# Kernel optimization log

Measured on AMD Instinct MI355X. Metric: run time of the kernel, lower is better.

The kernel has to match this reference:

```python
import jax, jax.numpy as jnp
import numpy as np

D_MODEL = 1024
N_HEAD = 16


def setup_inputs() -> dict:
    key = jax.random.key(0)
    ks = jax.random.split(key, 11)
    B, T, D = 4, 2048, D_MODEL
    s = 1.0 / np.sqrt(D)
    inp = {
        "q": jax.random.normal(ks[0], (B, T, D), jnp.float32),
        "k": jax.random.normal(ks[1], (B, T, D), jnp.float32),
        "v": jax.random.normal(ks[2], (B, T, D), jnp.float32),
        "wq": jax.random.normal(ks[3], (D, D), jnp.float32) * s,
        "bq": jnp.zeros((D,), jnp.float32),
        "wk": jax.random.normal(ks[4], (D, D), jnp.float32) * s,
        "bk": jnp.zeros((D,), jnp.float32),
        "wv": jax.random.normal(ks[5], (D, D), jnp.float32) * s,
        "bv": jnp.zeros((D,), jnp.float32),
        "wo": jax.random.normal(ks[6], (D, D), jnp.float32) * s,
        "bo": jnp.zeros((D,), jnp.float32),
    }
    return inp


def reference(q, k, v, wq, bq, wk, bk, wv, bv, wo, bo):
    B, T, D = q.shape
    H = N_HEAD
    hd = D // H  # head dim
    # torch nn.Linear: y = x @ W.T + b
    qh = (q @ wq.T + bq).reshape(B, T, H, hd).transpose(0, 2, 1, 3)  # [B,H,T,hd]
    kh = (k @ wk.T + bk).reshape(B, T, H, hd).transpose(0, 2, 1, 3)
    vh = (v @ wv.T + bv).reshape(B, T, H, hd).transpose(0, 2, 1, 3)
    scale = 1.0 / jnp.sqrt(jnp.asarray(hd, qh.dtype))
    score = jnp.einsum("bhqd,bhkd->bhqk", qh, kh) * scale  # [B,H,T,T]
    causal = jnp.tril(jnp.ones((T, T), dtype=bool))
    score = jnp.where(causal, score, jnp.asarray(-jnp.inf, score.dtype))
    attn = jax.nn.softmax(score, axis=-1)
    out = jnp.einsum("bhqk,bhkd->bhqd", attn, vh)  # [B,H,T,hd]
    out = out.transpose(0, 2, 1, 3).reshape(B, T, D)
    return out @ wo.T + bo
```

## Files before the change

### kernel.cpp

```cpp
#include <hip/hip_runtime.h>
#include <hip/hip_bf16.h>

#define D_MODEL 1024
#define N_HEAD  16
#define HD      64
#define T_SEQ   2048
#define B_SZ    4
#define M_ROWS  (B_SZ * T_SEQ)

typedef __bf16 bf16;
typedef __bf16 bf16x4 __attribute__((ext_vector_type(4)));
typedef __bf16 bf16x8 __attribute__((ext_vector_type(8)));
typedef float  floatx4 __attribute__((ext_vector_type(4)));

__device__ __forceinline__ floatx4 fzero4() {
    floatx4 z = {0.f, 0.f, 0.f, 0.f};
    return z;
}

__device__ __forceinline__ void async_ld16(const void* g, void* l) {
    __builtin_amdgcn_global_load_lds(
        (const __attribute__((address_space(1))) void*)g,
        (__attribute__((address_space(3))) void*)l,
        16, 0, 0);
}

struct CvtArgs {
    const float* s[7];
    bf16* d[7];
    int n[7];
};

__global__ __launch_bounds__(256) void cvt7_kernel(CvtArgs a)
{
    const float* src = a.s[blockIdx.y];
    bf16* dst = a.d[blockIdx.y];
    int n8 = a.n[blockIdx.y];
    int i = blockIdx.x * blockDim.x + threadIdx.x;
    int stride = gridDim.x * blockDim.x;
    for (; i < n8; i += stride) {
        float4 x = ((const float4*)src)[2 * i];
        float4 y = ((const float4*)src)[2 * i + 1];
        bf16x8 o;
        o[0] = (bf16)x.x; o[1] = (bf16)x.y; o[2] = (bf16)x.z; o[3] = (bf16)x.w;
        o[4] = (bf16)y.x; o[5] = (bf16)y.y; o[6] = (bf16)y.z; o[7] = (bf16)y.w;
        ((bf16x8*)dst)[i] = o;
    }
}

template <int OMODE>
__global__ __launch_bounds__(256) void gemm_bf16(
    const bf16* __restrict__ A0, const bf16* __restrict__ W0,
    const float* __restrict__ b0v, void* __restrict__ O0, float scl0,
    const bf16* __restrict__ A1, const bf16* __restrict__ W1,
    const float* __restrict__ b1v, void* __restrict__ O1, float scl1)
{
    __shared__ bf16 ldsA[128 * 64];
    __shared__ bf16 ldsW[128 * 64];

    const bf16* A     = blockIdx.z ? A1 : A0;
    const bf16* W     = blockIdx.z ? W1 : W0;
    const float* bias = blockIdx.z ? b1v : b0v;
    void* Out         = blockIdx.z ? O1 : O0;
    const float scl   = blockIdx.z ? scl1 : scl0;

    const int tid  = threadIdx.x;
    const int wave = tid >> 6, lane = tid & 63;
    const int quad = lane >> 4, l15 = lane & 15;
    const int wr = wave >> 1, wc = wave & 1;
    const int m0 = blockIdx.y * 128, n0 = blockIdx.x * 128;

    floatx4 acc[4][4];
#pragma unroll
    for (int i = 0; i < 4; ++i)
#pragma unroll
        for (int j = 0; j < 4; ++j) acc[i][j] = fzero4();

    const int ro = lane >> 3;
    const int gc = (lane & 7) ^ ro;
    const bf16* gA = A + (size_t)(m0 + wave * 32 + ro) * 1024 + gc * 8;
    const bf16* gW = W + (size_t)(n0 + wave * 32 + ro) * 1024 + gc * 8;

    for (int kt = 0; kt < 16; ++kt) {
        __syncthreads();
#pragma unroll
        for (int j = 0; j < 4; ++j)
            async_ld16((const void*)(gA + kt * 64 + j * 8 * 1024), &ldsA[(wave * 32 + j * 8) * 64]);
#pragma unroll
        for (int j = 0; j < 4; ++j)
            async_ld16((const void*)(gW + kt * 64 + j * 8 * 1024), &ldsW[(wave * 32 + j * 8) * 64]);
        __syncthreads();

#pragma unroll
        for (int ks = 0; ks < 2; ++ks) {
            const int pos = ((ks * 4 + quad) ^ (l15 & 7)) * 8;
            bf16x8 af[4], bw[4];
#pragma unroll
            for (int i = 0; i < 4; ++i)
                af[i] = *(const bf16x8*)(&ldsA[(wr * 64 + i * 16 + l15) * 64 + pos]);
#pragma unroll
            for (int j = 0; j < 4; ++j)
                bw[j] = *(const bf16x8*)(&ldsW[(wc * 64 + j * 16 + l15) * 64 + pos]);
#pragma unroll
            for (int i = 0; i < 4; ++i)
#pragma unroll
                for (int j = 0; j < 4; ++j)
                    acc[i][j] = __builtin_amdgcn_mfma_f32_16x16x32_bf16(af[i], bw[j], acc[i][j], 0, 0, 0);
        }
    }

#pragma unroll
    for (int i = 0; i < 4; ++i) {
#pragma unroll
        for (int j = 0; j < 4; ++j) {
#pragma unroll
            for (int r = 0; r < 4; ++r) {
                int m = m0 + wr * 64 + i * 16 + quad * 4 + r;
                int n = n0 + wc * 64 + j * 16 + l15;
                float val = (acc[i][j][r] + bias[n]) * scl;
                if (OMODE == 2) {
                    ((float*)Out)[(size_t)m * 1024 + n] = val;
                } else {
                    int b = m >> 11, t = m & 2047;
                    int h = n >> 6,  d = n & 63;
                    size_t addr;
                    if (OMODE == 0)
                        addr = ((size_t)(b * N_HEAD + h) * T_SEQ + t) * HD + d;
                    else
                        addr = ((size_t)(b * N_HEAD + h) * HD + d) * T_SEQ + t;
                    ((bf16*)Out)[addr] = (bf16)val;
                }
            }
        }
    }
}

__global__ __launch_bounds__(256, 2) void attn_kernel(
    const bf16* __restrict__ Qh, const bf16* __restrict__ Kh,
    const bf16* __restrict__ Vt, bf16* __restrict__ AO)
{
    __shared__ bf16 Ks[128 * 64];
    __shared__ bf16 Vts[64 * 128];
    __shared__ bf16 Ps[128 * 72];

    const int tid  = threadIdx.x;
    const int wave = tid >> 6, lane = tid & 63;
    const int quad = lane >> 4, l15 = lane & 15;
    const int bh = blockIdx.y;
    const size_t base = (size_t)bh * T_SEQ * HD;
    const int bb = bh >> 4, hh = bh & 15;

    const int kro = lane >> 3;
    const int kgc = (lane & 7) ^ kro;
    const bf16* kgbase = Kh + base + (size_t)(wave * 32 + kro) * HD + kgc * 8;
    const int vrow_lo = lane >> 4;
    const int vchunk  = lane & 15;

    const bf16* vgbase[4];
    bf16* kdst[4];
    bf16* vdst[4];
#pragma unroll
    for (int j = 0; j < 4; ++j) {
        int d = wave * 16 + j * 4 + vrow_lo;
        int gcv = vchunk ^ (d & 15);
        vgbase[j] = Vt + base + (size_t)d * T_SEQ + gcv * 8;
        vdst[j]   = &Vts[d * 128 + vchunk * 8];
        kdst[j]   = &Ks[(wave * 32 + j * 8 + kro) * 64 + (lane & 7) * 8];
    }

    for (int phase = 0; phase < 2; ++phase) {
        const int qt = phase ? blockIdx.x : 15 - blockIdx.x;

        bf16x8 qf[2][2];
        const bf16* qbase = Qh + base + (size_t)(qt * 128 + wave * 32) * HD;
#pragma unroll
        for (int ti = 0; ti < 2; ++ti)
#pragma unroll
            for (int ks = 0; ks < 2; ++ks)
                qf[ti][ks] = *(const bf16x8*)(qbase + (ti * 16 + l15) * HD + ks * 32 + quad * 8);

        bf16x8 kreg[4], vreg[4];
#pragma unroll
        for (int j = 0; j < 4; ++j)
            kreg[j] = *(const bf16x8*)(kgbase + (size_t)(j * 8) * HD);
#pragma unroll
        for (int j = 0; j < 4; ++j)
            vreg[j] = *(const bf16x8*)(vgbase[j]);

        float mrow[2] = {-1e30f, -1e30f}, lrow[2] = {0.f, 0.f};
        floatx4 oacc[2][4];
#pragma unroll
        for (int ti = 0; ti < 2; ++ti)
#pragma unroll
            for (int nj = 0; nj < 4; ++nj) oacc[ti][nj] = fzero4();

        for (int kt = 0; kt <= qt; ++kt) {
            __syncthreads();
#pragma unroll
            for (int j = 0; j < 4; ++j) *(bf16x8*)kdst[j] = kreg[j];
#pragma unroll
            for (int j = 0; j < 4; ++j) *(bf16x8*)vdst[j] = vreg[j];
            __syncthreads();

            if (kt < qt) {
#pragma unroll
                for (int j = 0; j < 4; ++j)
                    kreg[j] = *(const bf16x8*)(kgbase + (size_t)((kt + 1) * 128 + j * 8) * HD);
#pragma unroll
                for (int j = 0; j < 4; ++j)
                    vreg[j] = *(const bf16x8*)(vgbase[j] + (kt + 1) * 128);
            }

            const bool diag = (kt == qt);
            const int lim = diag ? (2 * wave + 1) : 7;

            floatx4 sacc[2][8];
#pragma unroll
            for (int ti = 0; ti < 2; ++ti)
#pragma unroll
                for (int tj = 0; tj < 8; ++tj) sacc[ti][tj] = fzero4();
            __builtin_amdgcn_s_setprio(1);
#pragma unroll
            for (int ks = 0; ks < 2; ++ks) {
                const int pos = ((ks * 4 + quad) ^ (l15 & 7)) * 8;
#pragma unroll
                for (int tj = 0; tj < 8; ++tj) {
                    if (tj <= lim) {
                        bf16x8 kf = *(const bf16x8*)(&Ks[(tj * 16 + l15) * 64 + pos]);
                        sacc[0][tj] = __builtin_amdgcn_mfma_f32_16x16x32_bf16(kf, qf[0][ks], sacc[0][tj], 0, 0, 0);
                        sacc[1][tj] = __builtin_amdgcn_mfma_f32_16x16x32_bf16(kf, qf[1][ks], sacc[1][tj], 0, 0, 0);
                    }
                }
            }
            __builtin_amdgcn_s_setprio(0);

#pragma unroll
            for (int ti = 0; ti < 2; ++ti) {
                const int ql = wave * 32 + ti * 16 + l15;
                float mxp[4] = {-1e30f, -1e30f, -1e30f, -1e30f};
#pragma unroll
                for (int tj = 0; tj < 8; ++tj) {
                    if (tj <= lim) {
#pragma unroll
                        for (int r = 0; r < 4; ++r) {
                            float s = sacc[ti][tj][r];
                            if (diag && (tj * 16 + quad * 4 + r) > ql) s = -1e30f;
                            sacc[ti][tj][r] = s;
                            mxp[r] = fmaxf(mxp[r], s);
                        }
                    }
                }
                float mx = fmaxf(fmaxf(mxp[0], mxp[1]), fmaxf(mxp[2], mxp[3]));
                mx = fmaxf(mx, __shfl_xor(mx, 16));
                mx = fmaxf(mx, __shfl_xor(mx, 32));
                if (__any(mx > mrow[ti] + 8.0f)) {
                    float mnew  = fmaxf(mrow[ti], mx);
                    float alpha = exp2f(mrow[ti] - mnew);
                    mrow[ti] = mnew;
                    lrow[ti] *= alpha;
#pragma unroll
                    for (int r = 0; r < 4; ++r) {
                        float ar = __shfl(alpha, quad * 4 + r);
#pragma unroll
                        for (int nj = 0; nj < 4; ++nj)
                            oacc[ti][nj][r] *= ar;
                    }
                }
                float rs[4] = {0.f, 0.f, 0.f, 0.f};
#pragma unroll
                for (int tj = 0; tj < 8; ++tj) {
                    if (tj <= lim) {
#pragma unroll
                        for (int r = 0; r < 4; ++r) {
                            float p = exp2f(sacc[ti][tj][r] - mrow[ti]);
                            rs[r] += p;
                            sacc[ti][tj][r] = p;
                        }
                    }
                }
                float rsum = (rs[0] + rs[1]) + (rs[2] + rs[3]);
                rsum += __shfl_xor(rsum, 16);
                rsum += __shfl_xor(rsum, 32);
                lrow[ti] += rsum;
            }

#pragma unroll
            for (int h2 = 0; h2 < 2; ++h2) {
                if (4 * h2 > lim) break;
#pragma unroll
                for (int ti = 0; ti < 2; ++ti) {
                    const int ql = wave * 32 + ti * 16 + l15;
#pragma unroll
                    for (int tjo = 0; tjo < 4; ++tjo) {
                        int tj = 4 * h2 + tjo;
                        if (tj <= lim) {
                            bf16x4 pv;
#pragma unroll
                            for (int r = 0; r < 4; ++r) pv[r] = (bf16)sacc[ti][tj][r];
                            *(bf16x4*)(&Ps[ql * 72 + tjo * 16 + quad * 4]) = pv;
                        }
                    }
                }
#pragma unroll
                for (int ks2 = 0; ks2 < 2; ++ks2) {
                    const int gks = 2 * h2 + ks2;
                    if (diag && gks > wave) break;
                    bf16x8 pf[2];
                    pf[0] = *(const bf16x8*)(&Ps[(wave * 32 + l15) * 72 + ks2 * 32 + quad * 8]);
                    pf[1] = *(const bf16x8*)(&Ps[(wave * 32 + 16 + l15) * 72 + ks2 * 32 + quad * 8]);
                    __builtin_amdgcn_s_setprio(1);
#pragma unroll
                    for (int nj = 0; nj < 4; ++nj) {
                        int pos = ((gks * 4 + quad) ^ l15) * 8;
                        bf16x8 vf = *(const bf16x8*)(&Vts[(nj * 16 + l15) * 128 + pos]);
                        oacc[0][nj] = __builtin_amdgcn_mfma_f32_16x16x32_bf16(pf[0], vf, oacc[0][nj], 0, 0, 0);
                        oacc[1][nj] = __builtin_amdgcn_mfma_f32_16x16x32_bf16(pf[1], vf, oacc[1][nj], 0, 0, 0);
                    }
                    __builtin_amdgcn_s_setprio(0);
                }
            }
        }

#pragma unroll
        for (int ti = 0; ti < 2; ++ti) {
#pragma unroll
            for (int r = 0; r < 4; ++r) {
                float lv = __shfl(lrow[ti], quad * 4 + r);
                float rl = 1.f / lv;
                int qrow = qt * 128 + wave * 32 + ti * 16 + quad * 4 + r;
#pragma unroll
                for (int nj = 0; nj < 4; ++nj) {
                    int d = nj * 16 + l15;
                    AO[((size_t)(bb * T_SEQ + qrow)) * D_MODEL + hh * HD + d] =
                        (bf16)(oacc[ti][nj][r] * rl);
                }
            }
        }
    }
}

extern "C" void kernel_launch(void* const* d_in, const int* in_sizes, int n_in,
                              void* d_out, int out_size, void* d_ws, size_t ws_size,
                              hipStream_t stream)
{
    const float* q  = (const float*)d_in[0];
    const float* k  = (const float*)d_in[1];
    const float* v  = (const float*)d_in[2];
    const float* wq = (const float*)d_in[3];
    const float* bq = (const float*)d_in[4];
    const float* wk = (const float*)d_in[5];
    const float* bk = (const float*)d_in[6];
    const float* wv = (const float*)d_in[7];
    const float* bv = (const float*)d_in[8];
    const float* wo = (const float*)d_in[9];
    const float* bo = (const float*)d_in[10];

    char* ws  = (char*)d_ws;
    char* dob = (char*)d_out;
    const size_t MB = 1024 * 1024;

    bf16* Wqb = (bf16*)(ws);
    bf16* Wkb = (bf16*)(ws + 2 * MB);
    bf16* Wvb = (bf16*)(ws + 4 * MB);
    bf16* Vb  = (bf16*)(ws + 6 * MB);
    bf16* AO  = (bf16*)(ws + 6 * MB);
    bf16* Qh  = (bf16*)(ws + 22 * MB);
    bf16* Kh  = (bf16*)(ws + 38 * MB);
    bf16* Wob = (bf16*)(ws + 54 * MB);
    bf16* Qb  = (bf16*)(dob);
    bf16* Kb  = (bf16*)(dob + 16 * MB);
    bf16* Vt  = (bf16*)(dob);

    const int NQ8 = M_ROWS * D_MODEL / 8;
    const int NW8 = D_MODEL * D_MODEL / 8;
    const float QSCALE = 0.18033688011112042f;

    CvtArgs ca;
    ca.s[0] = q;  ca.d[0] = Qb;  ca.n[0] = NQ8;
    ca.s[1] = k;  ca.d[1] = Kb;  ca.n[1] = NQ8;
    ca.s[2] = v;  ca.d[2] = Vb;  ca.n[2] = NQ8;
    ca.s[3] = wq; ca.d[3] = Wqb; ca.n[3] = NW8;
    ca.s[4] = wk; ca.d[4] = Wkb; ca.n[4] = NW8;
    ca.s[5] = wv; ca.d[5] = Wvb; ca.n[5] = NW8;
    ca.s[6] = wo; ca.d[6] = Wob; ca.n[6] = NW8;

    hipLaunchKernelGGL(cvt7_kernel, dim3(512, 7), dim3(256), 0, stream, ca);
    hipLaunchKernelGGL((gemm_bf16<0>), dim3(8, 64, 2), dim3(256), 0, stream,
                       Qb, Wqb, bq, (void*)Qh, QSCALE,
                       Kb, Wkb, bk, (void*)Kh, 1.0f);
    hipLaunchKernelGGL((gemm_bf16<1>), dim3(8, 64, 1), dim3(256), 0, stream,
                       Vb, Wvb, bv, (void*)Vt, 1.0f,
                       Vb, Wvb, bv, (void*)Vt, 1.0f);
    hipLaunchKernelGGL(attn_kernel, dim3(8, 64), dim3(256), 0, stream, Qh, Kh, Vt, AO);
    hipLaunchKernelGGL((gemm_bf16<2>), dim3(8, 64, 1), dim3(256), 0, stream,
                       AO, Wob, bo, d_out, 1.0f,
                       AO, Wob, bo, d_out, 1.0f);
}
```

Before: 354.6 us.

## Fuse fp32-to-bf16 conversion into GEMM loads and merge QKV projections into one launch

Removes the standalone conversion kernel: the GEMMs now read fp32 activations and weights directly, convert them to bf16 in registers and store them into LDS. The Q, K and V projections are merged into a single launch with a grid z-dimension of 3. Global loads switch from async direct-to-LDS to register prefetch of the next k-tile, giving software pipelining. This avoids writing and re-reading bf16 copies of the inputs, but each GEMM block now reads fp32 data, twice the bytes of bf16, and weights are re-converted by every block that uses them.

```diff
diff --git a/kernel.cpp b/kernel.cpp
--- a/kernel.cpp
+++ b/kernel.cpp
@@ -18,51 +18,34 @@
     return z;
 }
 
-__device__ __forceinline__ void async_ld16(const void* g, void* l) {
-    __builtin_amdgcn_global_load_lds(
-        (const __attribute__((address_space(1))) void*)g,
-        (__attribute__((address_space(3))) void*)l,
-        16, 0, 0);
+__device__ __forceinline__ bf16x8 cvt8(const float4 a, const float4 b) {
+    bf16x8 o;
+    o[0] = (bf16)a.x; o[1] = (bf16)a.y; o[2] = (bf16)a.z; o[3] = (bf16)a.w;
+    o[4] = (bf16)b.x; o[5] = (bf16)b.y; o[6] = (bf16)b.z; o[7] = (bf16)b.w;
+    return o;
 }
 
-struct CvtArgs {
-    const float* s[7];
-    bf16* d[7];
-    int n[7];
+struct GemmArgs {
+    const void*  A[3];
+    const float* W[3];
+    const float* bias[3];
+    void*        Out[3];
+    float        scl[3];
+    int          omode[3];
 };
 
-__global__ __launch_bounds__(256) void cvt7_kernel(CvtArgs a)
-{
-    const float* src = a.s[blockIdx.y];
-    bf16* dst = a.d[blockIdx.y];
-    int n8 = a.n[blockIdx.y];
-    int i = blockIdx.x * blockDim.x + threadIdx.x;
-    int stride = gridDim.x * blockDim.x;
-    for (; i < n8; i += stride) {
-        float4 x = ((const float4*)src)[2 * i];
-        float4 y = ((const float4*)src)[2 * i + 1];
-        bf16x8 o;
-        o[0] = (bf16)x.x; o[1] = (bf16)x.y; o[2] = (bf16)x.z; o[3] = (bf16)x.w;
-        o[4] = (bf16)y.x; o[5] = (bf16)y.y; o[6] = (bf16)y.z; o[7] = (bf16)y.w;
-        ((bf16x8*)dst)[i] = o;
-    }
-}
-
-template <int OMODE>
-__global__ __launch_bounds__(256) void gemm_bf16(
-    const bf16* __restrict__ A0, const bf16* __restrict__ W0,
-    const float* __restrict__ b0v, void* __restrict__ O0, float scl0,
-    const bf16* __restrict__ A1, const bf16* __restrict__ W1,
-    const float* __restrict__ b1v, void* __restrict__ O1, float scl1)
+template <int AF32>
+__global__ __launch_bounds__(256, 2) void gemm_k(GemmArgs g)
 {
     __shared__ bf16 ldsA[128 * 64];
     __shared__ bf16 ldsW[128 * 64];
 
-    const bf16* A     = blockIdx.z ? A1 : A0;
-    const bf16* W     = blockIdx.z ? W1 : W0;
-    const float* bias = blockIdx.z ? b1v : b0v;
-    void* Out         = blockIdx.z ? O1 : O0;
-    const float scl   = blockIdx.z ? scl1 : scl0;
+    const int z = blockIdx.z;
+    const float* W    = g.W[z];
+    const float* bias = g.bias[z];
+    void* Out         = g.Out[z];
+    const float scl   = g.scl[z];
+    const int omode   = g.omode[z];
 
     const int tid  = threadIdx.x;
     const int wave = tid >> 6, lane = tid & 63;
@@ -77,19 +60,61 @@
         for (int j = 0; j < 4; ++j) acc[i][j] = fzero4();
 
     const int ro = lane >> 3;
-    const int gc = (lane & 7) ^ ro;
-    const bf16* gA = A + (size_t)(m0 + wave * 32 + ro) * 1024 + gc * 8;
-    const bf16* gW = W + (size_t)(n0 + wave * 32 + ro) * 1024 + gc * 8;
+    const int c8 = lane & 7;
+
+    bf16* dA = &ldsA[(wave * 32 + ro) * 64 + (c8 ^ ro) * 8];
+    bf16* dW = &ldsW[(wave * 32 + ro) * 64 + (c8 ^ ro) * 8];
+
+    const float* gW = W + (size_t)(n0 + wave * 32 + ro) * 1024 + c8 * 8;
+    const float* gAf = nullptr;
+    const bf16*  gAb = nullptr;
+    if constexpr (AF32)
+        gAf = (const float*)g.A[z] + (size_t)(m0 + wave * 32 + ro) * 1024 + c8 * 8;
+    else
+        gAb = (const bf16*)g.A[z] + (size_t)(m0 + wave * 32 + ro) * 1024 + c8 * 8;
+
+    float4 rw[4][2];
+    float4 raf[4][2];
+    bf16x8 rab[4];
+
+#pragma unroll
+    for (int j = 0; j < 4; ++j) {
+        if constexpr (AF32) {
+            raf[j][0] = *(const float4*)(gAf + (size_t)j * 8192);
+            raf[j][1] = *(const float4*)(gAf + (size_t)j * 8192 + 4);
+        } else {
+            rab[j] = *(const bf16x8*)(gAb + (size_t)j * 8192);
+        }
+        rw[j][0] = *(const float4*)(gW + (size_t)j * 8192);
+        rw[j][1] = *(const float4*)(gW + (size_t)j * 8192 + 4);
+    }
 
     for (int kt = 0; kt < 16; ++kt) {
         __syncthreads();
 #pragma unroll
-        for (int j = 0; j < 4; ++j)
-            async_ld16((const void*)(gA + kt * 64 + j * 8 * 1024), &ldsA[(wave * 32 + j * 8) * 64]);
-#pragma unroll
-        for (int j = 0; j < 4; ++j)
-            async_ld16((const void*)(gW + kt * 64 + j * 8 * 1024), &ldsW[(wave * 32 + j * 8) * 64]);
+        for (int j = 0; j < 4; ++j) {
+            if constexpr (AF32)
+                *(bf16x8*)(dA + j * 8 * 64) = cvt8(raf[j][0], raf[j][1]);
+            else
+                *(bf16x8*)(dA + j * 8 * 64) = rab[j];
+            *(bf16x8*)(dW + j * 8 * 64) = cvt8(rw[j][0], rw[j][1]);
+        }
         __syncthreads();
+
+        if (kt < 15) {
+            const int off = (kt + 1) * 64;
+#pragma unroll
+            for (int j = 0; j < 4; ++j) {
+                if constexpr (AF32) {
+                    raf[j][0] = *(const float4*)(gAf + off + (size_t)j * 8192);
+                    raf[j][1] = *(const float4*)(gAf + off + (size_t)j * 8192 + 4);
+                } else {
+                    rab[j] = *(const bf16x8*)(gAb + off + (size_t)j * 8192);
+                }
+                rw[j][0] = *(const float4*)(gW + off + (size_t)j * 8192);
+                rw[j][1] = *(const float4*)(gW + off + (size_t)j * 8192 + 4);
+            }
+        }
 
 #pragma unroll
         for (int ks = 0; ks < 2; ++ks) {
@@ -118,13 +143,13 @@
                 int m = m0 + wr * 64 + i * 16 + quad * 4 + r;
                 int n = n0 + wc * 64 + j * 16 + l15;
                 float val = (acc[i][j][r] + bias[n]) * scl;
-                if (OMODE == 2) {
+                if (omode == 2) {
                     ((float*)Out)[(size_t)m * 1024 + n] = val;
                 } else {
                     int b = m >> 11, t = m & 2047;
                     int h = n >> 6,  d = n & 63;
                     size_t addr;
-                    if (OMODE == 0)
+                    if (omode == 0)
                         addr = ((size_t)(b * N_HEAD + h) * T_SEQ + t) * HD + d;
                     else
                         addr = ((size_t)(b * N_HEAD + h) * HD + d) * T_SEQ + t;
@@ -359,40 +384,24 @@
     char* dob = (char*)d_out;
     const size_t MB = 1024 * 1024;
 
-    bf16* Wqb = (bf16*)(ws);
-    bf16* Wkb = (bf16*)(ws + 2 * MB);
-    bf16* Wvb = (bf16*)(ws + 4 * MB);
-    bf16* Vb  = (bf16*)(ws + 6 * MB);
     bf16* AO  = (bf16*)(ws + 6 * MB);
     bf16* Qh  = (bf16*)(ws + 22 * MB);
     bf16* Kh  = (bf16*)(ws + 38 * MB);
-    bf16* Wob = (bf16*)(ws + 54 * MB);
-    bf16* Qb  = (bf16*)(dob);
-    bf16* Kb  = (bf16*)(dob + 16 * MB);
     bf16* Vt  = (bf16*)(dob);
 
-    const int NQ8 = M_ROWS * D_MODEL / 8;
-    const int NW8 = D_MODEL * D_MODEL / 8;
     const float QSCALE = 0.18033688011112042f;
 
-    CvtArgs ca;
-    ca.s[0] = q;  ca.d[0] = Qb;  ca.n[0] = NQ8;
-    ca.s[1] = k;  ca.d[1] = Kb;  ca.n[1] = NQ8;
-    ca.s[2] = v;  ca.d[2] = Vb;  ca.n[2] = NQ8;
-    ca.s[3] = wq; ca.d[3] = Wqb; ca.n[3] = NW8;
-    ca.s[4] = wk; ca.d[4] = Wkb; ca.n[4] = NW8;
-    ca.s[5] = wv; ca.d[5] = Wvb; ca.n[5] = NW8;
-    ca.s[6] = wo; ca.d[6] = Wob; ca.n[6] = NW8;
-
-    hipLaunchKernelGGL(cvt7_kernel, dim3(512, 7), dim3(256), 0, stream, ca);
-    hipLaunchKernelGGL((gemm_bf16<0>), dim3(8, 64, 2), dim3(256), 0, stream,
-                       Qb, Wqb, bq, (void*)Qh, QSCALE,
-                       Kb, Wkb, bk, (void*)Kh, 1.0f);
-    hipLaunchKernelGGL((gemm_bf16<1>), dim3(8, 64, 1), dim3(256), 0, stream,
-                       Vb, Wvb, bv, (void*)Vt, 1.0f,
-                       Vb, Wvb, bv, (void*)Vt, 1.0f);
+    GemmArgs gq;
+    gq.A[0] = q; gq.W[0] = wq; gq.bias[0] = bq; gq.Out[0] = (void*)Qh; gq.scl[0] = QSCALE; gq.omode[0] = 0;
+    gq.A[1] = k; gq.W[1] = wk; gq.bias[1] = bk; gq.Out[1] = (void*)Kh; gq.scl[1] = 1.0f;   gq.omode[1] = 0;
+    gq.A[2] = v; gq.W[2] = wv; gq.bias[2] = bv; gq.Out[2] = (void*)Vt; gq.scl[2] = 1.0f;   gq.omode[2] = 1;
+
+    GemmArgs go;
+    go.A[0] = AO; go.W[0] = wo; go.bias[0] = bo; go.Out[0] = d_out; go.scl[0] = 1.0f; go.omode[0] = 2;
+    go.A[1] = AO; go.W[1] = wo; go.bias[1] = bo; go.Out[1] = d_out; go.scl[1] = 1.0f; go.omode[1] = 2;
+    go.A[2] = AO; go.W[2] = wo; go.bias[2] = bo; go.Out[2] = d_out; go.scl[2] = 1.0f; go.omode[2] = 2;
+
+    hipLaunchKernelGGL((gemm_k<1>), dim3(8, 64, 3), dim3(256), 0, stream, gq);
     hipLaunchKernelGGL(attn_kernel, dim3(8, 64), dim3(256), 0, stream, Qh, Kh, Vt, AO);
-    hipLaunchKernelGGL((gemm_bf16<2>), dim3(8, 64, 1), dim3(256), 0, stream,
-                       AO, Wob, bo, d_out, 1.0f,
-                       AO, Wob, bo, d_out, 1.0f);
+    hipLaunchKernelGGL((gemm_k<0>), dim3(8, 64, 1), dim3(256), 0, stream, go);
 }
```

Measured after the change: 450.0 us. 1.27x slower.

## Enlarge projection GEMM tiles to 256x128 with 8 waves and vectorize transposed V stores

Applied to the files above, without the earlier changes.

The templated 128x128 GEMM is replaced by a single 512-thread kernel that computes a 256x128 output tile. The output mode (head layout, transposed V layout, or fp32) is now chosen at runtime from an argument struct. Each W tile is now reused across twice as many A rows, and the block grid order is swapped so x walks M. In the transposed-V epilogue, the four row accumulators that are contiguous in t are packed into one bf16x4 store instead of four strided scalar stores. The cost is fewer blocks per launch (256 for the V and output projections), more LDS per block, and a runtime branch in the epilogue.

```diff
diff --git a/kernel.cpp b/kernel.cpp
--- a/kernel.cpp
+++ b/kernel.cpp
@@ -18,6 +18,13 @@
     return z;
 }
 
+__device__ __forceinline__ bf16x8 cvt8(const float4 a, const float4 b) {
+    bf16x8 o;
+    o[0] = (bf16)a.x; o[1] = (bf16)a.y; o[2] = (bf16)a.z; o[3] = (bf16)a.w;
+    o[4] = (bf16)b.x; o[5] = (bf16)b.y; o[6] = (bf16)b.z; o[7] = (bf16)b.w;
+    return o;
+}
+
 __device__ __forceinline__ void async_ld16(const void* g, void* l) {
     __builtin_amdgcn_global_load_lds(
         (const __attribute__((address_space(1))) void*)g,
@@ -30,7 +37,6 @@
     bf16* d[7];
     int n[7];
 };
-
 __global__ __launch_bounds__(256) void cvt7_kernel(CvtArgs a)
 {
     const float* src = a.s[blockIdx.y];
@@ -41,34 +47,37 @@
     for (; i < n8; i += stride) {
         float4 x = ((const float4*)src)[2 * i];
         float4 y = ((const float4*)src)[2 * i + 1];
-        bf16x8 o;
-        o[0] = (bf16)x.x; o[1] = (bf16)x.y; o[2] = (bf16)x.z; o[3] = (bf16)x.w;
-        o[4] = (bf16)y.x; o[5] = (bf16)y.y; o[6] = (bf16)y.z; o[7] = (bf16)y.w;
-        ((bf16x8*)dst)[i] = o;
+        ((bf16x8*)dst)[i] = cvt8(x, y);
     }
 }
 
-template <int OMODE>
-__global__ __launch_bounds__(256) void gemm_bf16(
-    const bf16* __restrict__ A0, const bf16* __restrict__ W0,
-    const float* __restrict__ b0v, void* __restrict__ O0, float scl0,
-    const bf16* __restrict__ A1, const bf16* __restrict__ W1,
-    const float* __restrict__ b1v, void* __restrict__ O1, float scl1)
+struct GemmArgs {
+    const bf16* A[2];
+    const bf16* W[2];
+    const float* bias[2];
+    void*       Out[2];
+    float       scl[2];
+    int         omode[2];
+};
+
+__global__ __launch_bounds__(512, 4) void gemm_k(GemmArgs g)
 {
-    __shared__ bf16 ldsA[128 * 64];
+    __shared__ bf16 ldsA[256 * 64];
     __shared__ bf16 ldsW[128 * 64];
 
-    const bf16* A     = blockIdx.z ? A1 : A0;
-    const bf16* W     = blockIdx.z ? W1 : W0;
-    const float* bias = blockIdx.z ? b1v : b0v;
-    void* Out         = blockIdx.z ? O1 : O0;
-    const float scl   = blockIdx.z ? scl1 : scl0;
+    const int z = blockIdx.z;
+    const bf16* A     = g.A[z];
+    const bf16* W     = g.W[z];
+    const float* bias = g.bias[z];
+    void* Out         = g.Out[z];
+    const float scl   = g.scl[z];
+    const int omode   = g.omode[z];
 
     const int tid  = threadIdx.x;
     const int wave = tid >> 6, lane = tid & 63;
     const int quad = lane >> 4, l15 = lane & 15;
     const int wr = wave >> 1, wc = wave & 1;
-    const int m0 = blockIdx.y * 128, n0 = blockIdx.x * 128;
+    const int m0 = blockIdx.x * 256, n0 = blockIdx.y * 128;
 
     floatx4 acc[4][4];
 #pragma unroll
@@ -77,18 +86,20 @@
         for (int j = 0; j < 4; ++j) acc[i][j] = fzero4();
 
     const int ro = lane >> 3;
-    const int gc = (lane & 7) ^ ro;
-    const bf16* gA = A + (size_t)(m0 + wave * 32 + ro) * 1024 + gc * 8;
-    const bf16* gW = W + (size_t)(n0 + wave * 32 + ro) * 1024 + gc * 8;
+    const int c8 = lane & 7;
+    const bf16* gA = A + (size_t)(m0 + wave * 32 + ro) * 1024 + (c8 ^ ro) * 8;
+    const bf16* gW = W + (size_t)(n0 + wave * 16 + ro) * 1024 + (c8 ^ ro) * 8;
 
     for (int kt = 0; kt < 16; ++kt) {
         __syncthreads();
 #pragma unroll
         for (int j = 0; j < 4; ++j)
-            async_ld16((const void*)(gA + kt * 64 + j * 8 * 1024), &ldsA[(wave * 32 + j * 8) * 64]);
-#pragma unroll
-        for (int j = 0; j < 4; ++j)
-            async_ld16((const void*)(gW + kt * 64 + j * 8 * 1024), &ldsW[(wave * 32 + j * 8) * 64]);
+            async_ld16((const void*)(gA + kt * 64 + (size_t)j * 8 * 1024),
+                       &ldsA[(wave * 32 + j * 8) * 64]);
+#pragma unroll
+        for (int j = 0; j < 2; ++j)
+            async_ld16((const void*)(gW + kt * 64 + (size_t)j * 8 * 1024),
+                       &ldsW[(wave * 16 + j * 8) * 64]);
         __syncthreads();
 
 #pragma unroll
@@ -113,22 +124,31 @@
     for (int i = 0; i < 4; ++i) {
 #pragma unroll
         for (int j = 0; j < 4; ++j) {
-#pragma unroll
-            for (int r = 0; r < 4; ++r) {
-                int m = m0 + wr * 64 + i * 16 + quad * 4 + r;
+            if (omode == 1) {
+                int m = m0 + wr * 64 + i * 16 + quad * 4;
                 int n = n0 + wc * 64 + j * 16 + l15;
-                float val = (acc[i][j][r] + bias[n]) * scl;
-                if (OMODE == 2) {
-                    ((float*)Out)[(size_t)m * 1024 + n] = val;
-                } else {
-                    int b = m >> 11, t = m & 2047;
-                    int h = n >> 6,  d = n & 63;
-                    size_t addr;
-                    if (OMODE == 0)
-                        addr = ((size_t)(b * N_HEAD + h) * T_SEQ + t) * HD + d;
-                    else
-                        addr = ((size_t)(b * N_HEAD + h) * HD + d) * T_SEQ + t;
-                    ((bf16*)Out)[addr] = (bf16)val;
+                int b = m >> 11, t0 = m & 2047;
+                int h = n >> 6,  d = n & 63;
+                bf16x4 pv;
+#pragma unroll
+                for (int r = 0; r < 4; ++r)
+                    pv[r] = (bf16)((acc[i][j][r] + bias[n]) * scl);
+                size_t addr = ((size_t)(b * N_HEAD + h) * HD + d) * T_SEQ + t0;
+                *(bf16x4*)(&((bf16*)Out)[addr]) = pv;
+            } else {
+#pragma unroll
+                for (int r = 0; r < 4; ++r) {
+                    int m = m0 + wr * 64 + i * 16 + quad * 4 + r;
+                    int n = n0 + wc * 64 + j * 16 + l15;
+                    float val = (acc[i][j][r] + bias[n]) * scl;
+                    if (omode == 2) {
+                        ((float*)Out)[(size_t)m * 1024 + n] = val;
+                    } else {
+                        int b = m >> 11, t = m & 2047;
+                        int h = n >> 6,  d = n & 63;
+                        size_t addr = ((size_t)(b * N_HEAD + h) * T_SEQ + t) * HD + d;
+                        ((bf16*)Out)[addr] = (bf16)val;
+                    }
                 }
             }
         }
@@ -362,11 +382,11 @@
     bf16* Wqb = (bf16*)(ws);
     bf16* Wkb = (bf16*)(ws + 2 * MB);
     bf16* Wvb = (bf16*)(ws + 4 * MB);
-    bf16* Vb  = (bf16*)(ws + 6 * MB);
-    bf16* AO  = (bf16*)(ws + 6 * MB);
-    bf16* Qh  = (bf16*)(ws + 22 * MB);
-    bf16* Kh  = (bf16*)(ws + 38 * MB);
-    bf16* Wob = (bf16*)(ws + 54 * MB);
+    bf16* Wob = (bf16*)(ws + 6 * MB);
+    bf16* Vb  = (bf16*)(ws + 8 * MB);
+    bf16* AO  = (bf16*)(ws + 8 * MB);
+    bf16* Qh  = (bf16*)(ws + 24 * MB);
+    bf16* Kh  = (bf16*)(ws + 40 * MB);
     bf16* Qb  = (bf16*)(dob);
     bf16* Kb  = (bf16*)(dob + 16 * MB);
     bf16* Vt  = (bf16*)(dob);
@@ -384,15 +404,21 @@
     ca.s[5] = wv; ca.d[5] = Wvb; ca.n[5] = NW8;
     ca.s[6] = wo; ca.d[6] = Wob; ca.n[6] = NW8;
 
+    GemmArgs gqk;
+    gqk.A[0] = Qb; gqk.W[0] = Wqb; gqk.bias[0] = bq; gqk.Out[0] = (void*)Qh; gqk.scl[0] = QSCALE; gqk.omode[0] = 0;
+    gqk.A[1] = Kb; gqk.W[1] = Wkb; gqk.bias[1] = bk; gqk.Out[1] = (void*)Kh; gqk.scl[1] = 1.0f;   gqk.omode[1] = 0;
+
+    GemmArgs gv;
+    gv.A[0] = Vb; gv.W[0] = Wvb; gv.bias[0] = bv; gv.Out[0] = (void*)Vt; gv.scl[0] = 1.0f; gv.omode[0] = 1;
+    gv.A[1] = Vb; gv.W[1] = Wvb; gv.bias[1] = bv; gv.Out[1] = (void*)Vt; gv.scl[1] = 1.0f; gv.omode[1] = 1;
+
+    GemmArgs go;
+    go.A[0] = AO; go.W[0] = Wob; go.bias[0] = bo; go.Out[0] = d_out; go.scl[0] = 1.0f; go.omode[0] = 2;
+    go.A[1] = AO; go.W[1] = Wob; go.bias[1] = bo; go.Out[1] = d_out; go.scl[1] = 1.0f; go.omode[1] = 2;
+
     hipLaunchKernelGGL(cvt7_kernel, dim3(512, 7), dim3(256), 0, stream, ca);
-    hipLaunchKernelGGL((gemm_bf16<0>), dim3(8, 64, 2), dim3(256), 0, stream,
-                       Qb, Wqb, bq, (void*)Qh, QSCALE,
-                       Kb, Wkb, bk, (void*)Kh, 1.0f);
-    hipLaunchKernelGGL((gemm_bf16<1>), dim3(8, 64, 1), dim3(256), 0, stream,
-                       Vb, Wvb, bv, (void*)Vt, 1.0f,
-                       Vb, Wvb, bv, (void*)Vt, 1.0f);
+    hipLaunchKernelGGL(gemm_k, dim3(32, 8, 2), dim3(512), 0, stream, gqk);
+    hipLaunchKernelGGL(gemm_k, dim3(32, 8, 1), dim3(512), 0, stream, gv);
     hipLaunchKernelGGL(attn_kernel, dim3(8, 64), dim3(256), 0, stream, Qh, Kh, Vt, AO);
-    hipLaunchKernelGGL((gemm_bf16<2>), dim3(8, 64, 1), dim3(256), 0, stream,
-                       AO, Wob, bo, d_out, 1.0f,
-                       AO, Wob, bo, d_out, 1.0f);
-}
+    hipLaunchKernelGGL(gemm_k, dim3(32, 8, 1), dim3(512), 0, stream, go);
+}
```

After: 351.7 us. About the same (-0.8%).
